# Optimization experiments

Measured on AMD Instinct MI355X. Metric: run time of the kernel, lower is better.

Reference implementation:

```python
import jax, jax.numpy as jnp
import numpy as np

B, S, H = 8, 1024, 768
NUM_HEADS, DH = 12, 64
A, T = 12, 64

def setup_inputs() -> dict:
    key = jax.random.key(0)
    ks = jax.random.split(key, 12)
    all_tokens = jax.random.normal(ks[0], (B, S, H), dtype=jnp.float32)
    aspect_tokens = jax.random.normal(ks[1], (B, A, H), dtype=jnp.float32)
    # ragged target slices: start in [0, S-17), length in [1, 16]
    starts = jax.random.randint(ks[2], (T,), 0, S - 17)
    lens = jax.random.randint(ks[3], (T,), 1, 17)
    target_pos_info = jnp.stack([starts, starts + lens], axis=-1).astype(jnp.int32)  # (T,2)
    target_batch_info = jnp.sort(jax.random.randint(ks[4], (T,), 0, B)).astype(jnp.int32)
    attention_mask = jnp.ones((B, S), dtype=jnp.int32)
    s = 0.02
    W1 = jax.random.normal(ks[5], (H, H), dtype=jnp.float32) * s
    b1 = jnp.zeros((H,), dtype=jnp.float32)
    Wq = jax.random.normal(ks[6], (H, NUM_HEADS, DH), dtype=jnp.float32) * s
    bq = jnp.zeros((NUM_HEADS, DH), dtype=jnp.float32)
    Wk = jax.random.normal(ks[7], (H, NUM_HEADS, DH), dtype=jnp.float32) * s
    bk = jnp.zeros((NUM_HEADS, DH), dtype=jnp.float32)
    Wc = jax.random.normal(ks[8], (2 * H, 1), dtype=jnp.float32) * s
    bc = jnp.zeros((1,), dtype=jnp.float32)
    return {"all_tokens": all_tokens, "aspect_tokens": aspect_tokens,
            "target_pos_info": target_pos_info, "target_batch_info": target_batch_info,
            "attention_mask": attention_mask,
            "W1": W1, "b1": b1, "Wq": Wq, "bq": bq, "Wk": Wk, "bk": bk,
            "Wc": Wc, "bc": bc}


def reference(all_tokens, aspect_tokens, target_pos_info, target_batch_info,
              attention_mask, W1, b1, Wq, bq, Wk, bk, Wc, bc):
    # linear_transform (shared for tokens and aspects), dropout = identity at eval
    h = jax.nn.relu(jnp.einsum('bsh,hg->bsg', all_tokens, W1) + b1)     # (B,S,H)
    # SelfAttention: q/k EinsumDense projections; value = raw key_states reshaped
    q = jnp.einsum('bsh,hkd->bskd', h, Wq) + bq                          # (B,S,K,D)
    k = jnp.einsum('bsh,hkd->bskd', h, Wk) + bk
    v = h.reshape(k.shape)                                               # faithful: reshape, no proj
    q = q * jax.lax.rsqrt(jnp.asarray(DH, q.dtype))
    scores = jnp.einsum('bskd,bqkd->bkqs', k, q)                         # (B,K,Q,S)
    mask_val = attention_mask[:, 0].astype(scores.dtype)                 # original uses mask[:, 0:1]
    scores = scores + ((1.0 - mask_val) * -10000.0)[:, None, None, None]
    probs = jax.nn.softmax(scores, axis=-1)
    out = jnp.einsum('bkqs,bskd->bqkd', probs, v).reshape(h.shape)       # (B,S,H)
    # ragged per-target slice mean: masked mean over positions [s0, s1)
    pos = jnp.arange(S)
    s0, s1 = target_pos_info[:, 0], target_pos_info[:, 1]
    span = ((pos[None, :] >= s0[:, None]) & (pos[None, :] < s1[:, None])).astype(out.dtype)  # (T,S)
    gathered = out[target_batch_info]                                    # (T,S,H)
    counts = jnp.maximum(span.sum(-1, keepdims=True), 1.0)
    rep = jnp.einsum('ts,tsh->th', span, gathered) / counts              # (T,H)
    # aspect hidden states and target-aspect pairing (batch-ordered concat)
    h_a = jax.nn.relu(jnp.einsum('bah,hg->bag', aspect_tokens, W1) + b1)  # (B,A,H)
    pair = jnp.concatenate([jnp.broadcast_to(rep[:, None, :], (rep.shape[0], A, H)),
                            h_a[target_batch_info]], axis=-1)             # (T,A,2H)
    t_a_logit = jnp.einsum('tac,co->tao', pair, Wc) + bc                  # (T,A,1)
    return t_a_logit
```

## Files before the change

### kernel.cpp

```cpp
#include <hip/hip_runtime.h>


typedef __attribute__((ext_vector_type(8))) short s8v;
typedef __attribute__((ext_vector_type(4))) short s4v;
typedef __attribute__((ext_vector_type(4))) float f4v;

#define AS1 __attribute__((address_space(1)))
#define AS3 __attribute__((address_space(3)))

__device__ __forceinline__ unsigned short f2bf(float f) {
  union { float f; unsigned u; } v; v.f = f;
  unsigned r = v.u + 0x7FFFu + ((v.u >> 16) & 1u);
  return (unsigned short)(r >> 16);
}

__device__ __forceinline__ float bf2f(unsigned short u) {
  union { unsigned u; float f; } v; v.u = ((unsigned)u) << 16;
  return v.f;
}

__device__ __forceinline__ void gl2lds16(const void* g, void* l) {
  __builtin_amdgcn_global_load_lds((const AS1 void*)g, (AS3 void*)l, 16, 0, 0);
}

__global__ __launch_bounds__(256) void k_prep(const float* __restrict__ X,
                                              const float* __restrict__ asp,
                                              const float* __restrict__ W1,
                                              const float* __restrict__ Wq,
                                              const float* __restrict__ Wk,
                                              unsigned short* __restrict__ Xbf,
                                              unsigned short* __restrict__ Abf,
                                              unsigned short* __restrict__ W1t,
                                              unsigned short* __restrict__ Wqt,
                                              unsigned short* __restrict__ Wkt) {
  __shared__ float T[64][68];
  int bid = blockIdx.x;
  int tid = threadIdx.x;
  if (bid < 3072) {
    int i = bid * 256 + tid;
    const float4* src = (const float4*)(X + (size_t)i * 8);
    float4 a = src[0], b = src[1];
    s8v o;
    o[0] = (short)f2bf(a.x); o[1] = (short)f2bf(a.y);
    o[2] = (short)f2bf(a.z); o[3] = (short)f2bf(a.w);
    o[4] = (short)f2bf(b.x); o[5] = (short)f2bf(b.y);
    o[6] = (short)f2bf(b.z); o[7] = (short)f2bf(b.w);
    *(s8v*)(Xbf + (size_t)i * 8) = o;
  } else if (bid < 3108) {
    int i = (bid - 3072) * 256 + tid;
    const float4* src = (const float4*)(asp + (size_t)i * 8);
    float4 a = src[0], b = src[1];
    s8v o;
    o[0] = (short)f2bf(a.x); o[1] = (short)f2bf(a.y);
    o[2] = (short)f2bf(a.z); o[3] = (short)f2bf(a.w);
    o[4] = (short)f2bf(b.x); o[5] = (short)f2bf(b.y);
    o[6] = (short)f2bf(b.z); o[7] = (short)f2bf(b.w);
    *(s8v*)(Abf + (size_t)i * 8) = o;
  } else {
    int wb = bid - 3108;
    const float* W = (wb < 144) ? W1 : (wb < 288) ? Wq : Wk;
    unsigned short* Wt = (wb < 144) ? W1t : (wb < 288) ? Wqt : Wkt;
    int tile = wb % 144;
    int tr = (tile / 12) * 64;
    int tc = (tile % 12) * 64;
#pragma unroll
    for (int p = 0; p < 4; ++p) {
      int r = p * 16 + (tid >> 4);
      int c = (tid & 15) * 4;
      float4 v = *(const float4*)(W + (size_t)(tr + r) * 768 + tc + c);
      T[r][c] = v.x; T[r][c + 1] = v.y; T[r][c + 2] = v.z; T[r][c + 3] = v.w;
    }
    __syncthreads();
#pragma unroll
    for (int p = 0; p < 2; ++p) {
      int n = p * 32 + (tid >> 3);
      int k8 = (tid & 7) * 8;
      s8v o;
#pragma unroll
      for (int j = 0; j < 8; ++j) o[j] = (short)f2bf(T[k8 + j][n]);
      *(s8v*)(Wt + (size_t)(tc + n) * 768 + tr + k8) = o;
    }
  }
}

template <int MODE>
__device__ __forceinline__ void gemm_tile(int m0, int n0,
    const unsigned short* __restrict__ A, const unsigned short* __restrict__ Bt,
    const float* __restrict__ bias, unsigned short* __restrict__ C,
    unsigned short* __restrict__ C2, const int* __restrict__ pos,
    const int* __restrict__ tbi, unsigned short* As, unsigned short* Bs,
    int* srcRow) {
  const int K = 768;
  int tid = threadIdx.x, lane = tid & 63, w = tid >> 6;

  if (MODE == 2) {
    if (tid < 64) {
      int r = m0 + tid;
      int t = r >> 4, j = r & 15;
      int s0 = pos[2 * t], s1 = pos[2 * t + 1];
      int s = s0 + j; if (s > s1 - 1) s = s1 - 1;
      srcRow[tid] = tbi[t] * 1024 + s;
    }
    __syncthreads();
  }

  int rsub = lane >> 3;
  int cXor = ((lane & 7) ^ rsub) * 8;
  const unsigned short* aSrc[2];
  const unsigned short* bSrc[4];
#pragma unroll
  for (int i = 0; i < 2; ++i) {
    int lr = (w * 2 + i) * 8 + rsub;
    size_t grow;
    if (MODE == 2) grow = (size_t)srcRow[lr];
    else if (MODE == 3) { int rr = m0 + lr; grow = (size_t)(rr < 96 ? rr : 95); }
    else grow = (size_t)(m0 + lr);
    aSrc[i] = A + grow * K + cXor;
  }
#pragma unroll
  for (int i = 0; i < 4; ++i) {
    int lr = (w * 4 + i) * 8 + rsub;
    bSrc[i] = Bt + (size_t)(n0 + lr) * K + cXor;
  }

  f4v acc[2][4];
#pragma unroll
  for (int i = 0; i < 2; ++i)
#pragma unroll
    for (int j = 0; j < 4; ++j) acc[i][j] = (f4v)(0.0f);

  int wm = (w >> 1) * 32, wn = (w & 1) * 64;
  int lc = lane & 15, lg = lane >> 4;
  int aIdx[2][2], bIdx[4][2];
#pragma unroll
  for (int mi = 0; mi < 2; ++mi) {
    int ra = wm + mi * 16 + lc;
#pragma unroll
    for (int kk = 0; kk < 2; ++kk)
      aIdx[mi][kk] = ra * 64 + (((kk * 4 + lg) ^ (ra & 7)) * 8);
  }
#pragma unroll
  for (int ni = 0; ni < 4; ++ni) {
    int rb = wn + ni * 16 + lc;
#pragma unroll
    for (int kk = 0; kk < 2; ++kk)
      bIdx[ni][kk] = rb * 64 + (((kk * 4 + lg) ^ (rb & 7)) * 8);
  }

  for (int k0 = 0; k0 < K; k0 += 64) {
#pragma unroll
    for (int i = 0; i < 2; ++i) gl2lds16(aSrc[i] + k0, As + (w * 2 + i) * 512);
#pragma unroll
    for (int i = 0; i < 4; ++i) gl2lds16(bSrc[i] + k0, Bs + (w * 4 + i) * 512);
    __syncthreads();
#pragma unroll
    for (int kk = 0; kk < 2; ++kk) {
      s8v ar[2], br[4];
#pragma unroll
      for (int mi = 0; mi < 2; ++mi) ar[mi] = *(const s8v*)(As + aIdx[mi][kk]);
#pragma unroll
      for (int ni = 0; ni < 4; ++ni) br[ni] = *(const s8v*)(Bs + bIdx[ni][kk]);
#pragma unroll
      for (int mi = 0; mi < 2; ++mi)
#pragma unroll
        for (int ni = 0; ni < 4; ++ni)
          acc[mi][ni] = __builtin_amdgcn_mfma_f32_16x16x32_bf16(ar[mi], br[ni], acc[mi][ni], 0, 0, 0);
    }
    __syncthreads();
  }

#pragma unroll
  for (int mi = 0; mi < 2; ++mi) {
#pragma unroll
    for (int ni = 0; ni < 4; ++ni) {
      int col = n0 + wn + ni * 16 + lc;
      float bv = bias[col];
      int row0 = m0 + wm + mi * 16 + lg * 4;
      if (MODE == 0) {
        s4v pk;
#pragma unroll
        for (int r = 0; r < 4; ++r) {
          float x = acc[mi][ni][r] + bv;
          x = x > 0.f ? x : 0.f;
          unsigned short h = f2bf(x);
          pk[r] = (short)h;
          C[(size_t)(row0 + r) * 768 + col] = h;
        }
        int b = row0 >> 10, s = row0 & 1023;
        int kh = col >> 6, d = col & 63;
        *(s4v*)(C2 + ((size_t)((b * 12 + kh) * 64 + d)) * 1024 + s) = pk;
      } else if (MODE == 1) {
#pragma unroll
        for (int r = 0; r < 4; ++r) {
          int row = row0 + r;
          float x = acc[mi][ni][r] + bv;
          int b = row >> 10, s = row & 1023;
          int kh = col >> 6, d = col & 63;
          C[(size_t)((b * 12 + kh) * 1024 + s) * 64 + d] = f2bf(x);
        }
      } else if (MODE == 2) {
#pragma unroll
        for (int r = 0; r < 4; ++r) {
          int row = row0 + r;
          float x = (acc[mi][ni][r] + bv) * 0.125f;
          int t = row >> 4, j = row & 15;
          int kh = col >> 6, d = col & 63;
          C[(size_t)((t * 12 + kh) * 16 + j) * 64 + d] = f2bf(x);
        }
      } else {
#pragma unroll
        for (int r = 0; r < 4; ++r) {
          int row = row0 + r;
          float x = acc[mi][ni][r] + bv;
          x = x > 0.f ? x : 0.f;
          if (row < 96) C[(size_t)row * 768 + col] = f2bf(x);
        }
      }
    }
  }
}

__global__ __launch_bounds__(256) void k_gemmA(const unsigned short* __restrict__ Xbf,
                                               const unsigned short* __restrict__ Abf,
                                               const unsigned short* __restrict__ W1t,
                                               const float* __restrict__ b1,
                                               unsigned short* __restrict__ Hbf,
                                               unsigned short* __restrict__ Vt,
                                               unsigned short* __restrict__ Ha) {
  __shared__ unsigned short As[64 * 64];
  __shared__ unsigned short Bs[128 * 64];
  __shared__ int srcRow[64];
  int bid = blockIdx.x;
  if (bid < 768) {
    bid = (bid & 7) * 96 + (bid >> 3);
    gemm_tile<0>((bid / 6) * 64, (bid % 6) * 128, Xbf, W1t, b1, Hbf, Vt,
                 (const int*)nullptr, (const int*)nullptr, As, Bs, srcRow);
  } else {
    int b2 = bid - 768;
    gemm_tile<3>((b2 / 6) * 64, (b2 % 6) * 128, Abf, W1t, b1, Ha,
                 (unsigned short*)nullptr, (const int*)nullptr, (const int*)nullptr,
                 As, Bs, srcRow);
  }
}

__global__ __launch_bounds__(256) void k_gemmB(const unsigned short* __restrict__ Hbf,
                                               const unsigned short* __restrict__ Wkt,
                                               const float* __restrict__ bk,
                                               unsigned short* __restrict__ Khm,
                                               const unsigned short* __restrict__ Wqt,
                                               const float* __restrict__ bq,
                                               unsigned short* __restrict__ Qhm,
                                               const int* __restrict__ pos,
                                               const int* __restrict__ tbi) {
  __shared__ unsigned short As[64 * 64];
  __shared__ unsigned short Bs[128 * 64];
  __shared__ int srcRow[64];
  int bid = blockIdx.x;
  bid = (bid & 7) * 108 + (bid >> 3);
  if (bid < 768) {
    gemm_tile<1>((bid / 6) * 64, (bid % 6) * 128, Hbf, Wkt, bk, Khm,
                 (unsigned short*)nullptr, (const int*)nullptr, (const int*)nullptr,
                 As, Bs, srcRow);
  } else {
    int b2 = bid - 768;
    gemm_tile<2>((b2 / 6) * 64, (b2 % 6) * 128, Hbf, Wqt, bq, Qhm,
                 (unsigned short*)nullptr, pos, tbi, As, Bs, srcRow);
  }
}

__global__ __launch_bounds__(256) void k_attn(const unsigned short* __restrict__ q_hm,
                                              const unsigned short* __restrict__ k_hm,
                                              const unsigned short* __restrict__ vt,
                                              const unsigned short* __restrict__ ha,
                                              const int* __restrict__ pos,
                                              const int* __restrict__ tbi,
                                              const float* __restrict__ Wc,
                                              const float* __restrict__ bc,
                                              float* __restrict__ outp) {
  __shared__ unsigned short P[16 * 1032];
  __shared__ float O[4][16][64];
  __shared__ float rsbuf[4][16];
  __shared__ float inv_rs[16];
  __shared__ float hpart[4];
  __shared__ float rabuf;

  int bid = blockIdx.x;
  bid = (bid & 7) * 96 + (bid >> 3);
  int t = bid / 12, kh = bid % 12;
  int b = tbi[t];
  int s0 = pos[2 * t], s1 = pos[2 * t + 1];
  int len = s1 - s0;
  int tid = threadIdx.x, lane = tid & 63, w = tid >> 6;
  int lg = lane >> 4, lc = lane & 15;

  const unsigned short* qb = q_hm + (size_t)((t * 12 + kh) * 16) * 64;
  s8v a0 = *(const s8v*)(qb + (size_t)lc * 64 + lg * 8);
  s8v a1 = *(const s8v*)(qb + (size_t)lc * 64 + 32 + lg * 8);

  const unsigned short* kb = k_hm + (size_t)((b * 12 + kh) * 1024) * 64;
  float rs[4] = {0.f, 0.f, 0.f, 0.f};
  for (int it = 0; it < 16; ++it) {
    int sb = it * 64 + w * 16;
    s8v b0 = *(const s8v*)(kb + (size_t)(sb + lc) * 64 + lg * 8);
    s8v b1 = *(const s8v*)(kb + (size_t)(sb + lc) * 64 + 32 + lg * 8);
    f4v c = (f4v)(0.0f);
    c = __builtin_amdgcn_mfma_f32_16x16x32_bf16(a0, b0, c, 0, 0, 0);
    c = __builtin_amdgcn_mfma_f32_16x16x32_bf16(a1, b1, c, 0, 0, 0);
#pragma unroll
    for (int r = 0; r < 4; ++r) {
      float p = __expf(c[r]);
      rs[r] += p;
      P[(lg * 4 + r) * 1032 + sb + lc] = f2bf(p);
    }
  }
#pragma unroll
  for (int m = 1; m < 16; m <<= 1) {
#pragma unroll
    for (int r = 0; r < 4; ++r) rs[r] += __shfl_xor(rs[r], m, 64);
  }
  if (lc == 0) {
#pragma unroll
    for (int r = 0; r < 4; ++r) rsbuf[w][lg * 4 + r] = rs[r];
  }
  __syncthreads();
  if (tid < 16)
    inv_rs[tid] = 1.0f / (rsbuf[0][tid] + rsbuf[1][tid] + rsbuf[2][tid] + rsbuf[3][tid]);

  const unsigned short* vb = vt + (size_t)((b * 12 + kh) * 64) * 1024;
  f4v oc[4];
#pragma unroll
  for (int n = 0; n < 4; ++n) oc[n] = (f4v)(0.0f);
  for (int it = 0; it < 8; ++it) {
    int s32 = it * 128 + w * 32;
    s8v pa = *(const s8v*)(P + lc * 1032 + s32 + lg * 8);
#pragma unroll
    for (int n = 0; n < 4; ++n) {
      s8v vbf = *(const s8v*)(vb + (size_t)(n * 16 + lc) * 1024 + s32 + lg * 8);
      oc[n] = __builtin_amdgcn_mfma_f32_16x16x32_bf16(pa, vbf, oc[n], 0, 0, 0);
    }
  }
#pragma unroll
  for (int n = 0; n < 4; ++n)
#pragma unroll
    for (int r = 0; r < 4; ++r) O[w][lg * 4 + r][n * 16 + lc] = oc[n][r];
  __syncthreads();
  if (w == 0) {
    float sum = 0.f;
    for (int j = 0; j < len; ++j) {
      float v = O[0][j][lane] + O[1][j][lane] + O[2][j][lane] + O[3][j][lane];
      sum += v * inv_rs[j];
    }
    float repd = sum / (float)len;
    float pr = repd * Wc[kh * 64 + lane];
#pragma unroll
    for (int m = 1; m < 64; m <<= 1) pr += __shfl_xor(pr, m, 64);
    if (lane == 0) rabuf = pr;
  } else {
    const unsigned short* hr = ha + (size_t)(b * 12 + kh) * 768;
    float p2 = 0.f;
#pragma unroll
    for (int q = 0; q < 4; ++q) {
      int g = (tid - 64) + q * 192;
      p2 += bf2f(hr[g]) * Wc[768 + g];
    }
#pragma unroll
    for (int m = 1; m < 64; m <<= 1) p2 += __shfl_xor(p2, m, 64);
    if (lane == 0) hpart[w] = p2;
  }
  __syncthreads();
  if (tid < 12) {
    float ra = rabuf;
    float had = hpart[1] + hpart[2] + hpart[3];
    float v = ra + ((tid == kh) ? (had + bc[0]) : 0.f);
    atomicAdd(&outp[t * 12 + tid], v);
  }
}

extern "C" void kernel_launch(void* const* d_in, const int* in_sizes, int n_in,
                              void* d_out, int out_size, void* d_ws, size_t ws_size,
                              hipStream_t stream) {
  const float* all_tokens = (const float*)d_in[0];
  const float* aspect     = (const float*)d_in[1];
  const int*   pos        = (const int*)d_in[2];
  const int*   tbi        = (const int*)d_in[3];
  const float* W1 = (const float*)d_in[5];
  const float* b1 = (const float*)d_in[6];
  const float* Wq = (const float*)d_in[7];
  const float* bq = (const float*)d_in[8];
  const float* Wk = (const float*)d_in[9];
  const float* bk = (const float*)d_in[10];
  const float* Wc = (const float*)d_in[11];
  const float* bc = (const float*)d_in[12];
  float* out = (float*)d_out;

  char* ws = (char*)d_ws;
  unsigned short* Xbf = (unsigned short*)(ws);
  unsigned short* W1t = (unsigned short*)(ws + 12582912);
  unsigned short* Wqt = (unsigned short*)(ws + 13762560);
  unsigned short* Wkt = (unsigned short*)(ws + 14942208);
  unsigned short* Hbf = (unsigned short*)(ws + 16121856);
  unsigned short* Khm = (unsigned short*)(ws + 28704768);
  unsigned short* Vt  = (unsigned short*)(ws + 41287680);
  unsigned short* Qhm = (unsigned short*)(ws + 53870592);
  unsigned short* Abf = (unsigned short*)(ws + 55640448);
  unsigned short* Ha  = (unsigned short*)(ws + 55787904);

  hipMemsetAsync(out, 0, (size_t)out_size * sizeof(float), stream);
  hipLaunchKernelGGL(k_prep, dim3(3540), dim3(256), 0, stream,
                     all_tokens, aspect, W1, Wq, Wk, Xbf, Abf, W1t, Wqt, Wkt);
  hipLaunchKernelGGL(k_gemmA, dim3(780), dim3(256), 0, stream,
                     Xbf, Abf, W1t, b1, Hbf, Vt, Ha);
  hipLaunchKernelGGL(k_gemmB, dim3(864), dim3(256), 0, stream,
                     Hbf, Wkt, bk, Khm, Wqt, bq, Qhm, pos, tbi);
  hipLaunchKernelGGL(k_attn, dim3(768), dim3(256), 0, stream,
                     Qhm, Khm, Vt, Ha, pos, tbi, Wc, bc, out);
}
```

Measured before the change: 84.77 us.

## Fuse fp32-to-bf16 activation conversion into first GEMM and fold output zeroing into prep

The separate pass that converted all_tokens and aspect tokens to bf16 is removed. The first GEMM now loads fp32 A tiles directly, converts them in registers and stores them to LDS, which avoids writing and rereading a 12 MB bf16 copy. The hipMemsetAsync on the output is replaced by an extra block in the prep kernel that zeroes the output. The cost is that A tiles now take a synchronous register path instead of async global-to-LDS loads, so less load latency may be hidden in the GEMM. The aspect tokens are still converted to bf16 in prep even though nothing reads that copy any more.

```diff
diff --git a/kernel.cpp b/kernel.cpp
--- a/kernel.cpp
+++ b/kernel.cpp
@@ -23,31 +23,20 @@
   __builtin_amdgcn_global_load_lds((const AS1 void*)g, (AS3 void*)l, 16, 0, 0);
 }
 
-__global__ __launch_bounds__(256) void k_prep(const float* __restrict__ X,
-                                              const float* __restrict__ asp,
+__global__ __launch_bounds__(256) void k_prep(const float* __restrict__ asp,
                                               const float* __restrict__ W1,
                                               const float* __restrict__ Wq,
                                               const float* __restrict__ Wk,
-                                              unsigned short* __restrict__ Xbf,
                                               unsigned short* __restrict__ Abf,
                                               unsigned short* __restrict__ W1t,
                                               unsigned short* __restrict__ Wqt,
-                                              unsigned short* __restrict__ Wkt) {
+                                              unsigned short* __restrict__ Wkt,
+                                              float* __restrict__ outz) {
   __shared__ float T[64][68];
   int bid = blockIdx.x;
   int tid = threadIdx.x;
-  if (bid < 3072) {
+  if (bid < 36) {
     int i = bid * 256 + tid;
-    const float4* src = (const float4*)(X + (size_t)i * 8);
-    float4 a = src[0], b = src[1];
-    s8v o;
-    o[0] = (short)f2bf(a.x); o[1] = (short)f2bf(a.y);
-    o[2] = (short)f2bf(a.z); o[3] = (short)f2bf(a.w);
-    o[4] = (short)f2bf(b.x); o[5] = (short)f2bf(b.y);
-    o[6] = (short)f2bf(b.z); o[7] = (short)f2bf(b.w);
-    *(s8v*)(Xbf + (size_t)i * 8) = o;
-  } else if (bid < 3108) {
-    int i = (bid - 3072) * 256 + tid;
     const float4* src = (const float4*)(asp + (size_t)i * 8);
     float4 a = src[0], b = src[1];
     s8v o;
@@ -56,8 +45,8 @@
     o[4] = (short)f2bf(b.x); o[5] = (short)f2bf(b.y);
     o[6] = (short)f2bf(b.z); o[7] = (short)f2bf(b.w);
     *(s8v*)(Abf + (size_t)i * 8) = o;
-  } else {
-    int wb = bid - 3108;
+  } else if (bid < 468) {
+    int wb = bid - 36;
     const float* W = (wb < 144) ? W1 : (wb < 288) ? Wq : Wk;
     unsigned short* Wt = (wb < 144) ? W1t : (wb < 288) ? Wqt : Wkt;
     int tile = wb % 144;
@@ -80,12 +69,16 @@
       for (int j = 0; j < 8; ++j) o[j] = (short)f2bf(T[k8 + j][n]);
       *(s8v*)(Wt + (size_t)(tc + n) * 768 + tr + k8) = o;
     }
-  }
-}
-
-template <int MODE>
+  } else {
+#pragma unroll
+    for (int q = 0; q < 3; ++q) outz[tid + q * 256] = 0.f;
+  }
+}
+
+template <int MODE, bool AF32>
 __device__ __forceinline__ void gemm_tile(int m0, int n0,
-    const unsigned short* __restrict__ A, const unsigned short* __restrict__ Bt,
+    const unsigned short* __restrict__ A, const float* __restrict__ Af,
+    const unsigned short* __restrict__ Bt,
     const float* __restrict__ bias, unsigned short* __restrict__ C,
     unsigned short* __restrict__ C2, const int* __restrict__ pos,
     const int* __restrict__ tbi, unsigned short* As, unsigned short* Bs,
@@ -107,6 +100,7 @@
   int rsub = lane >> 3;
   int cXor = ((lane & 7) ^ rsub) * 8;
   const unsigned short* aSrc[2];
+  const float* aSrcF[2];
   const unsigned short* bSrc[4];
 #pragma unroll
   for (int i = 0; i < 2; ++i) {
@@ -115,7 +109,8 @@
     if (MODE == 2) grow = (size_t)srcRow[lr];
     else if (MODE == 3) { int rr = m0 + lr; grow = (size_t)(rr < 96 ? rr : 95); }
     else grow = (size_t)(m0 + lr);
-    aSrc[i] = A + grow * K + cXor;
+    if (AF32) aSrcF[i] = Af + grow * K + cXor;
+    else aSrc[i] = A + grow * K + cXor;
   }
 #pragma unroll
   for (int i = 0; i < 4; ++i) {
@@ -149,9 +144,24 @@
 
   for (int k0 = 0; k0 < K; k0 += 64) {
 #pragma unroll
-    for (int i = 0; i < 2; ++i) gl2lds16(aSrc[i] + k0, As + (w * 2 + i) * 512);
-#pragma unroll
     for (int i = 0; i < 4; ++i) gl2lds16(bSrc[i] + k0, Bs + (w * 4 + i) * 512);
+    if (AF32) {
+#pragma unroll
+      for (int i = 0; i < 2; ++i) {
+        const float* p = aSrcF[i] + k0;
+        float4 v0 = *(const float4*)p;
+        float4 v1 = *(const float4*)(p + 4);
+        s8v o;
+        o[0] = (short)f2bf(v0.x); o[1] = (short)f2bf(v0.y);
+        o[2] = (short)f2bf(v0.z); o[3] = (short)f2bf(v0.w);
+        o[4] = (short)f2bf(v1.x); o[5] = (short)f2bf(v1.y);
+        o[6] = (short)f2bf(v1.z); o[7] = (short)f2bf(v1.w);
+        *(s8v*)(As + (w * 2 + i) * 512 + lane * 8) = o;
+      }
+    } else {
+#pragma unroll
+      for (int i = 0; i < 2; ++i) gl2lds16(aSrc[i] + k0, As + (w * 2 + i) * 512);
+    }
     __syncthreads();
 #pragma unroll
     for (int kk = 0; kk < 2; ++kk) {
@@ -220,8 +230,8 @@
   }
 }
 
-__global__ __launch_bounds__(256) void k_gemmA(const unsigned short* __restrict__ Xbf,
-                                               const unsigned short* __restrict__ Abf,
+__global__ __launch_bounds__(256) void k_gemmA(const float* __restrict__ X,
+                                               const float* __restrict__ asp,
                                                const unsigned short* __restrict__ W1t,
                                                const float* __restrict__ b1,
                                                unsigned short* __restrict__ Hbf,
@@ -233,13 +243,14 @@
   int bid = blockIdx.x;
   if (bid < 768) {
     bid = (bid & 7) * 96 + (bid >> 3);
-    gemm_tile<0>((bid / 6) * 64, (bid % 6) * 128, Xbf, W1t, b1, Hbf, Vt,
-                 (const int*)nullptr, (const int*)nullptr, As, Bs, srcRow);
+    gemm_tile<0, true>((bid / 6) * 64, (bid % 6) * 128, (const unsigned short*)nullptr,
+                       X, W1t, b1, Hbf, Vt, (const int*)nullptr, (const int*)nullptr,
+                       As, Bs, srcRow);
   } else {
     int b2 = bid - 768;
-    gemm_tile<3>((b2 / 6) * 64, (b2 % 6) * 128, Abf, W1t, b1, Ha,
-                 (unsigned short*)nullptr, (const int*)nullptr, (const int*)nullptr,
-                 As, Bs, srcRow);
+    gemm_tile<3, true>((b2 / 6) * 64, (b2 % 6) * 128, (const unsigned short*)nullptr,
+                       asp, W1t, b1, Ha, (unsigned short*)nullptr,
+                       (const int*)nullptr, (const int*)nullptr, As, Bs, srcRow);
   }
 }
 
@@ -258,13 +269,14 @@
   int bid = blockIdx.x;
   bid = (bid & 7) * 108 + (bid >> 3);
   if (bid < 768) {
-    gemm_tile<1>((bid / 6) * 64, (bid % 6) * 128, Hbf, Wkt, bk, Khm,
-                 (unsigned short*)nullptr, (const int*)nullptr, (const int*)nullptr,
-                 As, Bs, srcRow);
+    gemm_tile<1, false>((bid / 6) * 64, (bid % 6) * 128, Hbf, (const float*)nullptr,
+                        Wkt, bk, Khm, (unsigned short*)nullptr,
+                        (const int*)nullptr, (const int*)nullptr, As, Bs, srcRow);
   } else {
     int b2 = bid - 768;
-    gemm_tile<2>((b2 / 6) * 64, (b2 % 6) * 128, Hbf, Wqt, bq, Qhm,
-                 (unsigned short*)nullptr, pos, tbi, As, Bs, srcRow);
+    gemm_tile<2, false>((b2 / 6) * 64, (b2 % 6) * 128, Hbf, (const float*)nullptr,
+                        Wqt, bq, Qhm, (unsigned short*)nullptr, pos, tbi,
+                        As, Bs, srcRow);
   }
 }
 
@@ -394,7 +406,6 @@
   float* out = (float*)d_out;
 
   char* ws = (char*)d_ws;
-  unsigned short* Xbf = (unsigned short*)(ws);
   unsigned short* W1t = (unsigned short*)(ws + 12582912);
   unsigned short* Wqt = (unsigned short*)(ws + 13762560);
   unsigned short* Wkt = (unsigned short*)(ws + 14942208);
@@ -405,11 +416,10 @@
   unsigned short* Abf = (unsigned short*)(ws + 55640448);
   unsigned short* Ha  = (unsigned short*)(ws + 55787904);
 
-  hipMemsetAsync(out, 0, (size_t)out_size * sizeof(float), stream);
-  hipLaunchKernelGGL(k_prep, dim3(3540), dim3(256), 0, stream,
-                     all_tokens, aspect, W1, Wq, Wk, Xbf, Abf, W1t, Wqt, Wkt);
+  hipLaunchKernelGGL(k_prep, dim3(469), dim3(256), 0, stream,
+                     aspect, W1, Wq, Wk, Abf, W1t, Wqt, Wkt, out);
   hipLaunchKernelGGL(k_gemmA, dim3(780), dim3(256), 0, stream,
-                     Xbf, Abf, W1t, b1, Hbf, Vt, Ha);
+                     all_tokens, aspect, W1t, b1, Hbf, Vt, Ha);
   hipLaunchKernelGGL(k_gemmB, dim3(864), dim3(256), 0, stream,
                      Hbf, Wkt, bk, Khm, Wqt, bq, Qhm, pos, tbi);
   hipLaunchKernelGGL(k_attn, dim3(768), dim3(256), 0, stream,
```

After: 79.85 us. -5.8%, faster.
